# Kernel tuning notes

Hardware: AMD Instinct MI355X
Metric: run time of the kernel (lower is better)

The kernel has to match this reference:

```python
import jax, jax.numpy as jnp
import numpy as np

EPS = 1e-12  # torch.nn.functional.normalize default eps


def _l2norm(x, axis):
    n = jnp.sqrt(jnp.sum(x * x, axis=axis, keepdims=True))
    return x / jnp.maximum(n, EPS)


def setup_inputs() -> dict:
    key = jax.random.key(0)
    k1, k2 = jax.random.split(key)
    B, n_with_neg, neighbor, n_facet, emb_dim = 4096, 1, 128, 8, 16
    features = jax.random.normal(k1, (B, n_with_neg, n_facet * emb_dim), dtype=jnp.float32)
    metapath_features = jax.random.normal(
        k2, (B, n_with_neg, neighbor, n_facet * emb_dim), dtype=jnp.float32)
    return {
        "features": features,
        "metapath_features": metapath_features,
        "emb_dim": emb_dim,
        "n_facet": n_facet,
        "n_iter": 4,
    }


def reference(features, metapath_features, emb_dim, n_facet, n_iter):
    B, n = features.shape[0], features.shape[1]
    N = metapath_features.shape[2]
    # x: [B, n, F, D], z: [B, n, N, F, D]
    x = features.reshape(B, n, n_facet, emb_dim)
    z = metapath_features.reshape(B, n, N, n_facet, emb_dim)
    x = _l2norm(x, axis=3)
    z = _l2norm(z, axis=4)
    u = x
    for clus_iter in range(n_iter):
        # routing logits: dot over emb_dim -> [B, n, N, F]
        p = jnp.einsum('bnkfd,bnfd->bnkf', z, u)
        p = jax.nn.softmax(p, axis=3)
        # weighted sum over neighbors -> [B, n, F, D]
        u = jnp.einsum('bnkfd,bnkf->bnfd', z, p) + x
        if clus_iter < n_iter - 1:
            u = _l2norm(u, axis=3)
    return u.reshape(B, n_facet * emb_dim)
```

## Files before the change

### kernel.cpp

```cpp
#include <hip/hip_runtime.h>
#include <math.h>


#define CC 128
#define LOG2E 1.44269504088896340736f

typedef float f32x2 __attribute__((ext_vector_type(2)));
typedef unsigned u32x2 __attribute__((ext_vector_type(2)));

template<int CTRL>
__device__ __forceinline__ float dpp_add(float x) {
    int y = __builtin_amdgcn_update_dpp(0, __float_as_int(x), CTRL, 0xF, 0xF, true);
    return x + __int_as_float(y);
}
#define DPP_XOR1 0xB1
#define DPP_XOR2 0x4E
#define DPP_HMIR 0x141
#define DPP_MIR  0x140

__device__ __forceinline__ f32x2 xor16_add2(f32x2 v) {
    u32x2 r0 = __builtin_amdgcn_permlane16_swap(__float_as_uint(v.x), __float_as_uint(v.x), false, false);
    u32x2 r1 = __builtin_amdgcn_permlane16_swap(__float_as_uint(v.y), __float_as_uint(v.y), false, false);
    f32x2 o;
    o.x = __uint_as_float(r0.x) + __uint_as_float(r0.y);
    o.y = __uint_as_float(r1.x) + __uint_as_float(r1.y);
    return o;
}
__device__ __forceinline__ f32x2 xor32_add2(f32x2 v) {
    u32x2 r0 = __builtin_amdgcn_permlane32_swap(__float_as_uint(v.x), __float_as_uint(v.x), false, false);
    u32x2 r1 = __builtin_amdgcn_permlane32_swap(__float_as_uint(v.y), __float_as_uint(v.y), false, false);
    f32x2 o;
    o.x = __uint_as_float(r0.x) + __uint_as_float(r0.y);
    o.y = __uint_as_float(r1.x) + __uint_as_float(r1.y);
    return o;
}
__device__ __forceinline__ float rsq_guard(float s) {
    return __builtin_amdgcn_rsqf(fmaxf(s, 1e-24f));
}
__device__ __forceinline__ unsigned pack_bf16(float lo, float hi) {
    unsigned r;
    asm("v_cvt_pk_bf16_f32 %0, %1, %2" : "=v"(r) : "v"(lo), "v"(hi));
    return r;
}
__device__ __forceinline__ f32x2 unpack_bf16(unsigned u) {
    f32x2 r;
    r.x = __uint_as_float(u << 16);
    r.y = __uint_as_float(u & 0xFFFF0000u);
    return r;
}

__global__ __launch_bounds__(512, 8)
void hete_routing_kernel(const float* __restrict__ feat,
                         const float* __restrict__ mp,
                         float* __restrict__ out)
{
    __shared__ float part[8][CC];
    __shared__ float u_s[CC];

    const int t = threadIdx.x;
    const int wave = t >> 6;
    const int lane = t & 63;
    const int cg = lane & 15;
    const int kgl = lane >> 4;
    const int kq = wave * 4 + kgl;
    const int c0 = cg * 8;
    const int b = blockIdx.x;

    unsigned zp[4][4];
    {
        const float* zb = mp + (size_t)b * (128 * CC) + kq * 4 * CC + c0;
        float4 A[4], Bv[4];
#pragma unroll
        for (int kk = 0; kk < 4; ++kk) {
            A[kk]  = *reinterpret_cast<const float4*>(zb + kk * CC);
            Bv[kk] = *reinterpret_cast<const float4*>(zb + kk * CC + 4);
        }
#pragma unroll
        for (int kk = 0; kk < 4; ++kk) {
            float s = A[kk].x * A[kk].x + A[kk].y * A[kk].y
                    + A[kk].z * A[kk].z + A[kk].w * A[kk].w
                    + Bv[kk].x * Bv[kk].x + Bv[kk].y * Bv[kk].y
                    + Bv[kk].z * Bv[kk].z + Bv[kk].w * Bv[kk].w;
            s = dpp_add<DPP_XOR1>(s);
            const float inv = rsq_guard(s);
            zp[kk][0] = pack_bf16(A[kk].x * inv,  A[kk].y * inv);
            zp[kk][1] = pack_bf16(A[kk].z * inv,  A[kk].w * inv);
            zp[kk][2] = pack_bf16(Bv[kk].x * inv, Bv[kk].y * inv);
            zp[kk][3] = pack_bf16(Bv[kk].z * inv, Bv[kk].w * inv);
        }
    }

    float xh = 0.f;
    if (t < CC) {
        const float xv = feat[(size_t)b * CC + t];
        float s = xv * xv;
        s = dpp_add<DPP_XOR1>(s);
        s = dpp_add<DPP_XOR2>(s);
        s = dpp_add<DPP_HMIR>(s);
        s = dpp_add<DPP_MIR>(s);
        xh = xv * rsq_guard(s);
        u_s[t] = xh * LOG2E;
    }
    __syncthreads();

#pragma unroll
    for (int it = 0; it < 4; ++it) {
        f32x2 ur[4];
        {
            const float4 A  = *reinterpret_cast<const float4*>(&u_s[c0]);
            const float4 Bv = *reinterpret_cast<const float4*>(&u_s[c0 + 4]);
            ur[0] = f32x2{A.x, A.y};  ur[1] = f32x2{A.z, A.w};
            ur[2] = f32x2{Bv.x, Bv.y}; ur[3] = f32x2{Bv.z, Bv.w};
        }

        f32x2 pu[4] = {f32x2{0.f,0.f}, f32x2{0.f,0.f}, f32x2{0.f,0.f}, f32x2{0.f,0.f}};
#pragma unroll
        for (int kk = 0; kk < 4; ++kk) {
            const f32x2 z0 = unpack_bf16(zp[kk][0]);
            const f32x2 z1 = unpack_bf16(zp[kk][1]);
            const f32x2 z2 = unpack_bf16(zp[kk][2]);
            const f32x2 z3 = unpack_bf16(zp[kk][3]);
            f32x2 acc = z0 * ur[0];
            acc += z1 * ur[1];
            acc += z2 * ur[2];
            acc += z3 * ur[3];
            const float l = dpp_add<DPP_XOR1>(acc.x + acc.y);
            const float e = __builtin_amdgcn_exp2f(l);
            float su = dpp_add<DPP_XOR2>(e);
            su = dpp_add<DPP_HMIR>(su);
            su = dpp_add<DPP_MIR>(su);
            const float wk = e * __builtin_amdgcn_rcpf(su);
            const f32x2 ws = {wk, wk};
            pu[0] += z0 * ws;
            pu[1] += z1 * ws;
            pu[2] += z2 * ws;
            pu[3] += z3 * ws;
        }
#pragma unroll
        for (int j = 0; j < 4; ++j) {
            pu[j] = xor16_add2(pu[j]);
            pu[j] = xor32_add2(pu[j]);
        }
        if (kgl == 0) {
            float* dst = &part[wave][c0];
            *reinterpret_cast<float4*>(dst)     = make_float4(pu[0].x, pu[0].y, pu[1].x, pu[1].y);
            *reinterpret_cast<float4*>(dst + 4) = make_float4(pu[2].x, pu[2].y, pu[3].x, pu[3].y);
        }
        __syncthreads();

        if (t < CC) {
            float un = xh;
#pragma unroll
            for (int j = 0; j < 8; ++j) un += part[j][t];
            if (it < 3) {
                float s = un * un;
                s = dpp_add<DPP_XOR1>(s);
                s = dpp_add<DPP_XOR2>(s);
                s = dpp_add<DPP_HMIR>(s);
                s = dpp_add<DPP_MIR>(s);
                u_s[t] = un * rsq_guard(s) * LOG2E;
            } else {
                out[(size_t)b * CC + t] = un;
            }
        }
        if (it < 3) __syncthreads();
    }
}

extern "C" void kernel_launch(void* const* d_in, const int* in_sizes, int n_in,
                              void* d_out, int out_size, void* d_ws, size_t ws_size,
                              hipStream_t stream) {
    const float* feat = (const float*)d_in[0];
    const float* mp   = (const float*)d_in[1];
    float* out = (float*)d_out;
    const int B = in_sizes[0] / CC;
    hete_routing_kernel<<<B, 512, 0, stream>>>(feat, mp, out);
}
```

Before: 48.11 us.

## Replace per-iteration second barrier with double-buffered partials and redundant per-wave reduction

Every wave now reads all eight per-wave partial sums from a double-buffered shared array and reduces them redundantly with cross-lane swaps. Each wave then computes the normalized u in registers, so there is no broadcast through shared memory and no second __syncthreads per iteration. The x normalization is likewise computed redundantly in registers instead of by the first 128 threads. This trades some extra shared-memory reads and ALU work for one fewer barrier per iteration. Launch bounds drop from 8 to 6 waves per SIMD, giving the compiler more registers.

```diff
diff --git a/kernel.cpp b/kernel.cpp
--- a/kernel.cpp
+++ b/kernel.cpp
@@ -3,6 +3,8 @@
 
 
 #define CC 128
+#define ZSZ (128 * CC)
+#define PST 132
 #define LOG2E 1.44269504088896340736f
 
 typedef float f32x2 __attribute__((ext_vector_type(2)));
@@ -49,13 +51,12 @@
     return r;
 }
 
-__global__ __launch_bounds__(512, 8)
+__global__ __launch_bounds__(512, 6)
 void hete_routing_kernel(const float* __restrict__ feat,
                          const float* __restrict__ mp,
                          float* __restrict__ out)
 {
-    __shared__ float part[8][CC];
-    __shared__ float u_s[CC];
+    __shared__ float part[2][8][PST];
 
     const int t = threadIdx.x;
     const int wave = t >> 6;
@@ -68,7 +69,7 @@
 
     unsigned zp[4][4];
     {
-        const float* zb = mp + (size_t)b * (128 * CC) + kq * 4 * CC + c0;
+        const float* zb = mp + (size_t)b * ZSZ + kq * 4 * CC + c0;
         float4 A[4], Bv[4];
 #pragma unroll
         for (int kk = 0; kk < 4; ++kk) {
@@ -90,28 +91,29 @@
         }
     }
 
-    float xh = 0.f;
-    if (t < CC) {
-        const float xv = feat[(size_t)b * CC + t];
-        float s = xv * xv;
+    f32x2 xh[4], ur[4];
+    {
+        const float* px = feat + (size_t)b * CC + c0;
+        const float4 xa = *reinterpret_cast<const float4*>(px);
+        const float4 xc = *reinterpret_cast<const float4*>(px + 4);
+        xh[0] = f32x2{xa.x, xa.y}; xh[1] = f32x2{xa.z, xa.w};
+        xh[2] = f32x2{xc.x, xc.y}; xh[3] = f32x2{xc.z, xc.w};
+        f32x2 s2 = xh[0] * xh[0];
+        s2 += xh[1] * xh[1];
+        s2 += xh[2] * xh[2];
+        s2 += xh[3] * xh[3];
+        float s = s2.x + s2.y;
         s = dpp_add<DPP_XOR1>(s);
-        s = dpp_add<DPP_XOR2>(s);
-        s = dpp_add<DPP_HMIR>(s);
-        s = dpp_add<DPP_MIR>(s);
-        xh = xv * rsq_guard(s);
-        u_s[t] = xh * LOG2E;
+        const float inv = rsq_guard(s);
+        const f32x2 iv  = {inv, inv};
+        const f32x2 ivl = {inv * LOG2E, inv * LOG2E};
+#pragma unroll
+        for (int j = 0; j < 4; ++j) { ur[j] = xh[j] * ivl; xh[j] *= iv; }
     }
-    __syncthreads();
 
 #pragma unroll
     for (int it = 0; it < 4; ++it) {
-        f32x2 ur[4];
-        {
-            const float4 A  = *reinterpret_cast<const float4*>(&u_s[c0]);
-            const float4 Bv = *reinterpret_cast<const float4*>(&u_s[c0 + 4]);
-            ur[0] = f32x2{A.x, A.y};  ur[1] = f32x2{A.z, A.w};
-            ur[2] = f32x2{Bv.x, Bv.y}; ur[3] = f32x2{Bv.z, Bv.w};
-        }
+        const int p = it & 1;
 
         f32x2 pu[4] = {f32x2{0.f,0.f}, f32x2{0.f,0.f}, f32x2{0.f,0.f}, f32x2{0.f,0.f}};
 #pragma unroll
@@ -142,28 +144,48 @@
             pu[j] = xor32_add2(pu[j]);
         }
         if (kgl == 0) {
-            float* dst = &part[wave][c0];
+            float* dst = &part[p][wave][c0];
             *reinterpret_cast<float4*>(dst)     = make_float4(pu[0].x, pu[0].y, pu[1].x, pu[1].y);
             *reinterpret_cast<float4*>(dst + 4) = make_float4(pu[2].x, pu[2].y, pu[3].x, pu[3].y);
         }
         __syncthreads();
 
-        if (t < CC) {
-            float un = xh;
-#pragma unroll
-            for (int j = 0; j < 8; ++j) un += part[j][t];
-            if (it < 3) {
-                float s = un * un;
-                s = dpp_add<DPP_XOR1>(s);
-                s = dpp_add<DPP_XOR2>(s);
-                s = dpp_add<DPP_HMIR>(s);
-                s = dpp_add<DPP_MIR>(s);
-                u_s[t] = un * rsq_guard(s) * LOG2E;
-            } else {
-                out[(size_t)b * CC + t] = un;
-            }
-        }
-        if (it < 3) __syncthreads();
+        f32x2 un[4];
+        {
+            const float* r0 = &part[p][2 * kgl][c0];
+            const float* r1 = &part[p][2 * kgl + 1][c0];
+            const float4 a0 = *reinterpret_cast<const float4*>(r0);
+            const float4 a1 = *reinterpret_cast<const float4*>(r0 + 4);
+            const float4 b0 = *reinterpret_cast<const float4*>(r1);
+            const float4 b1 = *reinterpret_cast<const float4*>(r1 + 4);
+            un[0] = f32x2{a0.x + b0.x, a0.y + b0.y};
+            un[1] = f32x2{a0.z + b0.z, a0.w + b0.w};
+            un[2] = f32x2{a1.x + b1.x, a1.y + b1.y};
+            un[3] = f32x2{a1.z + b1.z, a1.w + b1.w};
+        }
+#pragma unroll
+        for (int j = 0; j < 4; ++j) {
+            un[j] = xor16_add2(un[j]);
+            un[j] = xor32_add2(un[j]);
+            un[j] += xh[j];
+        }
+
+        if (it < 3) {
+            f32x2 s2 = un[0] * un[0];
+            s2 += un[1] * un[1];
+            s2 += un[2] * un[2];
+            s2 += un[3] * un[3];
+            float s = s2.x + s2.y;
+            s = dpp_add<DPP_XOR1>(s);
+            const float ivl = rsq_guard(s) * LOG2E;
+            const f32x2 iv = {ivl, ivl};
+#pragma unroll
+            for (int j = 0; j < 4; ++j) ur[j] = un[j] * iv;
+        } else if (wave == 0 && kgl == 0) {
+            float* dst = out + (size_t)b * CC + c0;
+            *reinterpret_cast<float4*>(dst)     = make_float4(un[0].x, un[0].y, un[1].x, un[1].y);
+            *reinterpret_cast<float4*>(dst + 4) = make_float4(un[2].x, un[2].y, un[3].x, un[3].y);
+        }
     }
 }
 
```

After: 61.69 us. 28.2% more time.
